# Kernel tuning notes

Hardware: AMD Instinct MI355X
Metric: run time of the kernel (lower is better)

Reference implementation:

```python
import jax, jax.numpy as jnp
import numpy as np

B, D = 8192, 128
MARGIN = 0.1
N_CLASSES, N_GROUPS = 64, 8


def setup_inputs() -> dict:
    key = jax.random.key(0)
    k1, k2, k3 = jax.random.split(key, 3)
    embeddings = jax.random.normal(k1, (B, D), dtype=jnp.float32)
    labels = jax.random.randint(k2, (B,), 0, N_CLASSES, dtype=jnp.int64)
    groups = jax.random.randint(k3, (B,), 0, N_GROUPS, dtype=jnp.int64)
    return {"embeddings": embeddings, "labels": labels, "groups": groups}


def reference(embeddings, labels, groups):
    # cosine metric: L2-normalize rows (torch F.normalize eps=1e-12)
    norm = jnp.maximum(jnp.linalg.norm(embeddings, axis=1, keepdims=True), 1e-12)
    x = embeddings / norm
    dist = 1.0 - jnp.matmul(x, x.T)                      # [B, B]

    n = embeddings.shape[0]
    eye = jnp.eye(n, dtype=bool)
    same_label = labels[:, None] == labels[None, :]       # [B, B]
    pos_mask = same_label & ~eye
    neg_mask = ~same_label
    neg_sg_mask = neg_mask & (groups[:, None] == groups[None, :])

    BIG = jnp.float32(1e9)
    # hardest positive per row (masked max), hardest negative per row (masked min)
    dist_ap = jnp.max(jnp.where(pos_mask, dist, -BIG), axis=1)
    dist_an_sg = jnp.min(jnp.where(neg_sg_mask, dist, BIG), axis=1)
    dist_an_all = jnp.min(jnp.where(neg_mask, dist, BIG), axis=1)

    has_pos = jnp.any(pos_mask, axis=1)
    has_neg_sg = jnp.any(neg_sg_mask, axis=1)
    has_neg = jnp.any(neg_mask, axis=1)

    # fallback: same-group negatives preferred, else any negative
    dist_an = jnp.where(has_neg_sg, dist_an_sg, dist_an_all)

    loss = jax.nn.relu(dist_ap - dist_an + MARGIN)        # [B]
    # original only averages strictly-positive losses over valid anchors
    include = has_pos & has_neg & (loss > 0)
    cnt = jnp.sum(include.astype(jnp.float32))
    total = jnp.sum(jnp.where(include, loss, 0.0))
    final = jnp.where(cnt > 0, total / jnp.maximum(cnt, 1.0), 0.0)
    final = jnp.where(jnp.isnan(final), 0.0, final)
    return final
```

## Files before the change

### kernel.cpp

```cpp
#include <hip/hip_runtime.h>
#include <math.h>

#define NB 8192
#define DK 128
#define SPLITJ 16
#define JSPAN (NB / SPLITJ)
#define NJT (JSPAN / 32)
#define GRID_MINE ((NB / 128) * SPLITJ)

typedef __attribute__((ext_vector_type(8))) short short8;
typedef __attribute__((ext_vector_type(16))) float float16;

__device__ inline unsigned short f2bf(float f) {
    unsigned int x = __float_as_uint(f);
    unsigned int r = (x + 0x7fffu + ((x >> 16) & 1u)) >> 16;
    return (unsigned short)r;
}

__device__ inline unsigned enc_f(float f) {
    unsigned u = __float_as_uint(f);
    return ((int)u < 0) ? ~u : (u | 0x80000000u);
}
__device__ inline float dec_f(unsigned u) {
    unsigned b = (u & 0x80000000u) ? (u & 0x7fffffffu) : ~u;
    return __uint_as_float(b);
}

__device__ inline float biasf(int mi, int mj) {
    int x = mi ^ mj;
    bool sl = (unsigned)x < 16u;
    bool sg = (x & 15) == 0;
    float b0 = sg ? 4.0f : 0.0f;
    return sl ? -16.0f : b0;
}

__global__ void prep_kernel(const float* __restrict__ emb, const int* __restrict__ labels,
                            const int* __restrict__ groups, short8* __restrict__ frag,
                            int* __restrict__ meta, unsigned* __restrict__ apu,
                            unsigned* __restrict__ anu, int* __restrict__ ticket) {
    const int t   = blockIdx.x;
    const int tid = threadIdx.x;
    const int r   = tid >> 3;
    const int ks  = tid & 7;
    const int row = t * 32 + r;

    const float4* src = (const float4*)(emb + (size_t)row * DK + ks * 16);
    float4 q[4];
    float ss = 0.0f;
#pragma unroll
    for (int u = 0; u < 4; u++) {
        q[u] = src[u];
        ss += q[u].x * q[u].x + q[u].y * q[u].y + q[u].z * q[u].z + q[u].w * q[u].w;
    }
#pragma unroll
    for (int off = 4; off; off >>= 1) ss += __shfl_xor(ss, off, 64);
    float inv = 1.0f / fmaxf(sqrtf(ss), 1e-12f);

    unsigned short h[16];
#pragma unroll
    for (int u = 0; u < 4; u++) {
        h[u * 4 + 0] = f2bf(q[u].x * inv);
        h[u * 4 + 1] = f2bf(q[u].y * inv);
        h[u * 4 + 2] = f2bf(q[u].z * inv);
        h[u * 4 + 3] = f2bf(q[u].w * inv);
    }
    short8 lo, hi;
#pragma unroll
    for (int u = 0; u < 8; u++) { lo[u] = (short)h[u]; hi[u] = (short)h[8 + u]; }
    frag[(size_t)(t * 8 + ks) * 64 + r]      = lo;
    frag[(size_t)(t * 8 + ks) * 64 + 32 + r] = hi;

    if (ks == 0) meta[row] = (labels[row] << 4) | groups[row];
    if (ks == 1) apu[row] = 0xFFFFFFFFu;
    if (ks == 2) anu[row] = 0u;
    if (t == 0 && tid == 0) *ticket = 0;
}

__global__ __launch_bounds__(256, 2) void mine_mfma(
    const short8* __restrict__ frag, const int* __restrict__ meta,
    unsigned* __restrict__ apu, unsigned* __restrict__ anu,
    int* __restrict__ ticket, float* __restrict__ out) {
    const int tid  = threadIdx.x;
    const int w    = tid >> 6;
    const int lane = tid & 63;
    const int half = lane >> 5;
    const int l31  = lane & 31;
    const int irow  = blockIdx.y * 128 + w * 32;
    const int jbase = blockIdx.x * JSPAN;
    const int tA    = blockIdx.y * 4 + w;
    const int tB0   = blockIdx.x * NJT;

    short8 afrag[8];
#pragma unroll
    for (int ks = 0; ks < 8; ks++)
        afrag[ks] = frag[(size_t)(tA * 8 + ks) * 64 + lane];

    int metaI[16];
    float mn[16], mx[16];
#pragma unroll
    for (int reg = 0; reg < 16; reg++) {
        int r = (reg & 3) + 8 * (reg >> 2) + 4 * half;
        metaI[reg] = meta[irow + r];
        mn[reg] = 1e9f; mx[reg] = -1e9f;
    }

    short8  bb[2][8];
    float16 cc[2];

#pragma unroll
    for (int u = 0; u < 8; u++) bb[0][u] = frag[(size_t)(tB0 * 8 + u) * 64 + lane];
    {
        int mj = meta[jbase + l31];
#pragma unroll
        for (int reg = 0; reg < 16; reg++) cc[0][reg] = biasf(metaI[reg], mj);
    }

#pragma unroll 2
    for (int jt = 0; jt < NJT; jt++) {
        const int cur = jt & 1;

        if (jt + 1 < NJT) {
            const int tBn = tB0 + jt + 1;
#pragma unroll
            for (int u = 0; u < 8; u++)
                bb[cur ^ 1][u] = frag[(size_t)(tBn * 8 + u) * 64 + lane];
            int mjn = meta[jbase + (jt + 1) * 32 + l31];
#pragma unroll
            for (int reg = 0; reg < 16; reg++)
                cc[cur ^ 1][reg] = biasf(metaI[reg], mjn);
        }

#pragma unroll
        for (int u = 0; u < 8; u++)
            cc[cur] = __builtin_amdgcn_mfma_f32_32x32x16_bf16(afrag[u], bb[cur][u], cc[cur], 0, 0, 0);

#pragma unroll
        for (int reg = 0; reg < 16; reg++) {
            mn[reg] = fminf(mn[reg], cc[cur][reg]);
            mx[reg] = fmaxf(mx[reg], cc[cur][reg]);
        }
    }

#pragma unroll
    for (int reg = 0; reg < 16; reg++) {
#pragma unroll
        for (int off = 16; off; off >>= 1) {
            mn[reg] = fminf(mn[reg], __shfl_xor(mn[reg], off, 64));
            mx[reg] = fmaxf(mx[reg], __shfl_xor(mx[reg], off, 64));
        }
    }
    if (l31 == 0) {
#pragma unroll
        for (int reg = 0; reg < 16; reg++) {
            int r = (reg & 3) + 8 * (reg >> 2) + 4 * half;
            atomicMin(&apu[irow + r], enc_f(mn[reg]));
            atomicMax(&anu[irow + r], enc_f(mx[reg]));
        }
    }

    __shared__ float ssum[4], scnt[4];
    __shared__ int lastFlag;
    __syncthreads();
    if (tid == 0) {
        __threadfence();
        int old = atomicAdd(ticket, 1);
        lastFlag = (old == GRID_MINE - 1);
    }
    __syncthreads();
    if (!lastFlag) return;
    __threadfence();

    float s = 0.0f, ccnt = 0.0f;
#pragma unroll
    for (int k = 0; k < NB / 256; k++) {
        int i = tid + k * 256;
        float mnf = dec_f(apu[i]);
        float mxf = dec_f(anu[i]);
        float anS = (mxf > 2.0f) ? mxf - 4.0f : mxf;
        float loss = anS - mnf - 15.9f;
        if (loss > 0.0f) { s += loss; ccnt += 1.0f; }
    }
#pragma unroll
    for (int off = 32; off; off >>= 1) {
        s    += __shfl_xor(s, off, 64);
        ccnt += __shfl_xor(ccnt, off, 64);
    }
    if (lane == 0) { ssum[w] = s; scnt[w] = ccnt; }
    __syncthreads();
    if (tid == 0) {
        float ts = 0.f, tc = 0.f;
#pragma unroll
        for (int wv = 0; wv < 4; wv++) { ts += ssum[wv]; tc += scnt[wv]; }
        float r = (tc > 0.0f) ? ts / fmaxf(tc, 1.0f) : 0.0f;
        if (isnan(r)) r = 0.0f;
        out[0] = r;
    }
}

extern "C" void kernel_launch(void* const* d_in, const int* in_sizes, int n_in,
                              void* d_out, int out_size, void* d_ws, size_t ws_size,
                              hipStream_t stream) {
    const float* emb  = (const float*)d_in[0];
    const int* labels = (const int*)d_in[1];
    const int* groups = (const int*)d_in[2];
    float* out = (float*)d_out;

    short8*   fragp  = (short8*)d_ws;
    int*      meta   = (int*)((char*)d_ws + (size_t)NB * DK * 2);
    unsigned* apu    = (unsigned*)(meta + NB);
    unsigned* anu    = apu + NB;
    int*      ticket = (int*)(anu + NB);

    prep_kernel<<<NB / 32, 256, 0, stream>>>(emb, labels, groups, fragp, meta, apu, anu, ticket);
    mine_mfma<<<dim3(SPLITJ, NB / 128), 256, 0, stream>>>(fragp, meta, apu, anu, ticket, out);
}
```

Before: 111.3 us.

## Stage shared B tiles in LDS with double buffering across waves

Each block of four waves used to load the same B fragments from global memory into its own registers. Now the block loads 64-column B tiles cooperatively into a double-buffered LDS array, and each wave reads its MFMA operands from LDS. The j-split doubles to 32 and the occupancy hint rises to 3 blocks per SIMD. This cuts redundant global and L2 traffic and register pressure, but adds a block barrier on every tile and puts LDS read latency on the MFMA path.

```diff
diff --git a/kernel.cpp b/kernel.cpp
--- a/kernel.cpp
+++ b/kernel.cpp
@@ -3,9 +3,9 @@
 
 #define NB 8192
 #define DK 128
-#define SPLITJ 16
+#define SPLITJ 32
 #define JSPAN (NB / SPLITJ)
-#define NJT (JSPAN / 32)
+#define NT (JSPAN / 64)
 #define GRID_MINE ((NB / 128) * SPLITJ)
 
 typedef __attribute__((ext_vector_type(8))) short short8;
@@ -76,10 +76,12 @@
     if (t == 0 && tid == 0) *ticket = 0;
 }
 
-__global__ __launch_bounds__(256, 2) void mine_mfma(
+__global__ __launch_bounds__(256, 3) void mine_mfma(
     const short8* __restrict__ frag, const int* __restrict__ meta,
     unsigned* __restrict__ apu, unsigned* __restrict__ anu,
     int* __restrict__ ticket, float* __restrict__ out) {
+    __shared__ short8 Bs[2][1024];
+
     const int tid  = threadIdx.x;
     const int w    = tid >> 6;
     const int lane = tid & 63;
@@ -88,7 +90,7 @@
     const int irow  = blockIdx.y * 128 + w * 32;
     const int jbase = blockIdx.x * JSPAN;
     const int tA    = blockIdx.y * 4 + w;
-    const int tB0   = blockIdx.x * NJT;
+    const int tB0   = blockIdx.x * (JSPAN / 32);
 
     short8 afrag[8];
 #pragma unroll
@@ -104,41 +106,52 @@
         mn[reg] = 1e9f; mx[reg] = -1e9f;
     }
 
-    short8  bb[2][8];
-    float16 cc[2];
-
-#pragma unroll
-    for (int u = 0; u < 8; u++) bb[0][u] = frag[(size_t)(tB0 * 8 + u) * 64 + lane];
     {
-        int mj = meta[jbase + l31];
-#pragma unroll
-        for (int reg = 0; reg < 16; reg++) cc[0][reg] = biasf(metaI[reg], mj);
-    }
-
-#pragma unroll 2
-    for (int jt = 0; jt < NJT; jt++) {
+        const short8* src0 = frag + (size_t)(tB0 * 8) * 64;
+#pragma unroll
+        for (int s = 0; s < 4; s++) Bs[0][tid + s * 256] = src0[tid + s * 256];
+    }
+    __syncthreads();
+
+    for (int jt = 0; jt < NT; jt++) {
         const int cur = jt & 1;
-
-        if (jt + 1 < NJT) {
-            const int tBn = tB0 + jt + 1;
-#pragma unroll
-            for (int u = 0; u < 8; u++)
-                bb[cur ^ 1][u] = frag[(size_t)(tBn * 8 + u) * 64 + lane];
-            int mjn = meta[jbase + (jt + 1) * 32 + l31];
-#pragma unroll
-            for (int reg = 0; reg < 16; reg++)
-                cc[cur ^ 1][reg] = biasf(metaI[reg], mjn);
-        }
-
-#pragma unroll
-        for (int u = 0; u < 8; u++)
-            cc[cur] = __builtin_amdgcn_mfma_f32_32x32x16_bf16(afrag[u], bb[cur][u], cc[cur], 0, 0, 0);
-
-#pragma unroll
-        for (int reg = 0; reg < 16; reg++) {
-            mn[reg] = fminf(mn[reg], cc[cur][reg]);
-            mx[reg] = fmaxf(mx[reg], cc[cur][reg]);
-        }
+        const int j0  = jbase + jt * 64;
+
+        short8 pre[4];
+        if (jt + 1 < NT) {
+            const short8* srcn = frag + (size_t)((tB0 + (jt + 1) * 2) * 8) * 64;
+#pragma unroll
+            for (int s = 0; s < 4; s++) pre[s] = srcn[tid + s * 256];
+        }
+        int mjc[2];
+        mjc[0] = meta[j0 + l31];
+        mjc[1] = meta[j0 + 32 + l31];
+
+#pragma unroll
+        for (int ct = 0; ct < 2; ct++) {
+            const int mj = mjc[ct];
+            float16 c;
+#pragma unroll
+            for (int reg = 0; reg < 16; reg++) c[reg] = biasf(metaI[reg], mj);
+
+            const short8* base = &Bs[cur][ct * 512];
+#pragma unroll
+            for (int ks = 0; ks < 8; ks++) {
+                short8 b = base[ks * 64 + lane];
+                c = __builtin_amdgcn_mfma_f32_32x32x16_bf16(afrag[ks], b, c, 0, 0, 0);
+            }
+#pragma unroll
+            for (int reg = 0; reg < 16; reg++) {
+                mn[reg] = fminf(mn[reg], c[reg]);
+                mx[reg] = fmaxf(mx[reg], c[reg]);
+            }
+        }
+
+        if (jt + 1 < NT) {
+#pragma unroll
+            for (int s = 0; s < 4; s++) Bs[cur ^ 1][tid + s * 256] = pre[s];
+        }
+        __syncthreads();
     }
 
 #pragma unroll
```

Result: slower. 143.8 us (+29.2%).
